# Kernel optimization log

Measured on AMD Instinct MI355X. Metric: run time of the kernel, lower is better.

Reference implementation:

```python
import jax, jax.numpy as jnp
import numpy as np

N, E, D_IN, HID, OUT, EDIM, L, NT, ET = 50000, 800000, 128, 128, 128, 32, 3, 2, 3
PUMP = 1
LN_EPS = 1e-5


def setup_inputs() -> dict:
    key = jax.random.key(0)
    ks = jax.random.split(key, 12)
    s = 0.05
    x = jax.random.normal(ks[0], (N, D_IN), jnp.float32)
    edge_index = jax.random.randint(ks[1], (2, E), 0, N, dtype=jnp.int64)
    edge_attr = jax.random.normal(ks[2], (E, EDIM), jnp.float32)
    node_type = jax.random.randint(ks[3], (N,), 0, NT, dtype=jnp.int64)
    edge_type = jax.random.randint(ks[4], (E,), 0, ET, dtype=jnp.int64)
    # per-layer HydroConv params
    node_W = jax.random.normal(ks[5], (L, NT, HID, D_IN), jnp.float32) * s   # per-node-type Linear weight
    node_b = jax.random.normal(ks[6], (L, NT, HID), jnp.float32) * s
    edge_W = jax.random.normal(ks[7], (L, ET, 2, EDIM), jnp.float32) * s     # out dim padded to 2; row 1 only used for pump type
    edge_b = jax.random.normal(ks[8], (L, ET, 2), jnp.float32) * s
    emb = jax.random.normal(ks[9], (L, ET, EDIM), jnp.float32) * s           # edge_type_emb per layer
    ln_g = jnp.ones((L, HID), jnp.float32)
    ln_b = jnp.zeros((L, HID), jnp.float32)
    fc_W = jax.random.normal(ks[10], (OUT, HID), jnp.float32) * s
    fc_b = jnp.zeros((OUT,), jnp.float32)
    return dict(x=x, edge_attr=edge_attr, node_W=node_W, node_b=node_b,
                edge_W=edge_W, edge_b=edge_b, emb=emb, ln_g=ln_g, ln_b=ln_b,
                fc_W=fc_W, fc_b=fc_b, edge_index=edge_index,
                node_type=node_type, edge_type=edge_type)


def _hydro_conv(h, edge_index, edge_attr, node_type, edge_type, nW, nb, eW, eb, emb_l):
    src, dst = edge_index[0], edge_index[1]           # x_j = h[src], x_i = h[dst]
    direction = edge_attr[:, -2:-1]                    # [E,1]
    pump = edge_attr[:, -1:]                           # [E,1]
    ea = edge_attr + emb_l[edge_type]                  # [E,EDIM]
    raw = jnp.einsum('ec,toc->eto', ea, eW) + eb       # [E,ET,2]
    raw = jnp.take_along_axis(raw, edge_type[:, None, None], axis=1)[:, 0]  # [E,2] per-edge-type MLP
    gain = jax.nn.softplus(raw[:, :1])                 # [E,1]
    speed = pump * jnp.where(direction > 0, direction, jnp.ones_like(direction))
    is_pump = (edge_type == PUMP)[:, None]
    gain = jnp.where(is_pump, gain * speed, gain)
    bias = jnp.where(is_pump, raw[:, 1:2] * speed, jnp.zeros_like(gain))
    sign = direction * 2.0 - 1.0
    msg = sign * (gain * (h[src] - h[dst]) + bias)     # [E,C]
    aggr = jax.ops.segment_sum(msg, dst, num_segments=N)  # scatter-add to target nodes
    out = jnp.zeros((N, nW.shape[1]), h.dtype)
    for t in range(NT):                                # per-node-type Linear
        ht = aggr @ nW[t].T + nb[t]
        out = jnp.where((node_type == t)[:, None], ht, out)
    return out


def reference(x, edge_attr, node_W, node_b, edge_W, edge_b, emb, ln_g, ln_b,
              fc_W, fc_b, edge_index, node_type, edge_type):
    h = x
    for l in range(L):
        identity = h
        h = _hydro_conv(h, edge_index, edge_attr, node_type, edge_type,
                        node_W[l], node_b[l], edge_W[l], edge_b[l], emb[l])
        h = jax.nn.relu(h)
        mu = jnp.mean(h, axis=-1, keepdims=True)
        var = jnp.mean(jnp.square(h - mu), axis=-1, keepdims=True)
        h = (h - mu) * jax.lax.rsqrt(var + LN_EPS) * ln_g[l] + ln_b[l]
        if identity.shape == h.shape:                  # residual
            h = h + identity
    return h @ fc_W.T + fc_b
```

## Files before the change

kernel.cpp:

```cpp
#include <hip/hip_runtime.h>
#include <math.h>

#define NN 50000
#define EE 800000
#define D 128
#define EDIM 32
#define LL 3
#define NT 2
#define ET 3
#define NB 196
#define NPAD 50080
#define NTILE 1565
#define NBLKM 392

typedef _Float16 f16x8 __attribute__((ext_vector_type(8)));
typedef float f32x4 __attribute__((ext_vector_type(4)));

__device__ __forceinline__ void cvt8(const float4 u, const float4 v, f16x8& hi, f16x8& lo) {
    float x[8] = {u.x, u.y, u.z, u.w, v.x, v.y, v.z, v.w};
#pragma unroll
    for (int e = 0; e < 8; e++) {
        _Float16 h = (_Float16)x[e];
        hi[e] = h;
        lo[e] = (_Float16)(x[e] - (float)h);
    }
}

__global__ __launch_bounds__(256) void k_pcount(const int* __restrict__ nt, int* __restrict__ pc) {
    __shared__ int s[256];
    int d = blockIdx.x * 256 + threadIdx.x;
    int ind = 0;
    if (d < NN) ind = (nt[d] == 0) ? 1 : 0x10000;
    s[threadIdx.x] = ind;
    __syncthreads();
    for (int st = 128; st; st >>= 1) {
        if (threadIdx.x < st) s[threadIdx.x] += s[threadIdx.x + st];
        __syncthreads();
    }
    if (threadIdx.x == 0) pc[blockIdx.x] = s[0];
}

__global__ __launch_bounds__(256) void k_pscan(const int* __restrict__ pc, int* __restrict__ po,
                                               int* __restrict__ meta) {
    __shared__ int s[256];
    int t = threadIdx.x;
    int v = (t < NB) ? pc[t] : 0;
    s[t] = v;
    __syncthreads();
    for (int st = 1; st < 256; st <<= 1) {
        int add = (t >= st) ? s[t - st] : 0;
        __syncthreads();
        s[t] += add;
        __syncthreads();
    }
    if (t < NB) po[t] = s[t] - v;
    if (t == 0) {
        int tot = s[255];
        meta[3] = ((tot & 0xffff) + 63) & ~63;
    }
}

__global__ __launch_bounds__(256) void k_passign(const int* __restrict__ nt, const int* __restrict__ po,
                                                 const int* __restrict__ meta,
                                                 int* __restrict__ pos, int* __restrict__ inv) {
    __shared__ int s[256];
    int t = threadIdx.x;
    int d = blockIdx.x * 256 + t;
    int ty = (d < NN) ? nt[d] : -1;
    int ind = (ty == 0) ? 1 : ((ty == 1) ? 0x10000 : 0);
    s[t] = ind;
    __syncthreads();
    for (int st = 1; st < 256; st <<= 1) {
        int add = (t >= st) ? s[t - st] : 0;
        __syncthreads();
        s[t] += add;
        __syncthreads();
    }
    if (d >= NN) return;
    int excl = s[t] - ind;
    int pop = po[blockIdx.x];
    int p;
    if (ty == 0) p = (pop & 0xffff) + (excl & 0xffff);
    else         p = meta[3] + (pop >> 16) + (excl >> 16);
    pos[d] = p;
    inv[p] = d;
}

__global__ __launch_bounds__(256) void k_permx(const float* __restrict__ x, const int* __restrict__ pos,
                                               float* __restrict__ h0) {
    int flat = blockIdx.x * 256 + threadIdx.x;
    if (flat >= NN * 32) return;
    int d = flat >> 5, f4 = flat & 31;
    int p = pos[d];
    ((float4*)h0)[(size_t)p * 32 + f4] = ((const float4*)x)[(size_t)d * 32 + f4];
}

__global__ __launch_bounds__(256) void k_hist(const int* __restrict__ dst, int* __restrict__ deg) {
    int e = blockIdx.x * 256 + threadIdx.x;
    if (e < EE) atomicAdd(&deg[dst[e]], 1);
}

__global__ __launch_bounds__(256) void k_scan_bsum(const int* __restrict__ deg, int* __restrict__ bsum) {
    __shared__ int s[256];
    int t = threadIdx.x;
    int d = blockIdx.x * 256 + t;
    s[t] = (d < NN) ? deg[d] : 0;
    __syncthreads();
    for (int st = 128; st > 0; st >>= 1) {
        if (t < st) s[t] += s[t + st];
        __syncthreads();
    }
    if (t == 0) bsum[blockIdx.x] = s[0];
}

__global__ __launch_bounds__(256) void k_scan_boff(const int* __restrict__ bsum, int* __restrict__ boff) {
    __shared__ int s[256];
    int t = threadIdx.x;
    s[t] = (t < NB) ? bsum[t] : 0;
    __syncthreads();
    for (int st = 1; st < 256; st <<= 1) {
        int add = (t >= st) ? s[t - st] : 0;
        __syncthreads();
        s[t] += add;
        __syncthreads();
    }
    if (t < NB) boff[t] = (t == 0) ? 0 : s[t - 1];
}

__global__ __launch_bounds__(256) void k_scan_offs(const int* __restrict__ deg, const int* __restrict__ boff,
                                                   int* __restrict__ offs, int* __restrict__ cur) {
    __shared__ int s[256];
    int t = threadIdx.x;
    int d = blockIdx.x * 256 + t;
    int v = (d < NN) ? deg[d] : 0;
    s[t] = v;
    __syncthreads();
    for (int st = 1; st < 256; st <<= 1) {
        int add = (t >= st) ? s[t - st] : 0;
        __syncthreads();
        s[t] += add;
        __syncthreads();
    }
    if (d < NN) {
        int excl = s[t] - v + boff[blockIdx.x];
        offs[d] = excl;
        cur[d]  = excl;
    }
}

__global__ __launch_bounds__(256) void k_edge(const float* __restrict__ edge_attr,
                                              const float* __restrict__ edge_W,
                                              const float* __restrict__ edge_b,
                                              const float* __restrict__ emb,
                                              const int* __restrict__ ei,
                                              const int* __restrict__ etype,
                                              const int* __restrict__ pos,
                                              int* __restrict__ cur,
                                              float4* __restrict__ esort) {
    __shared__ float eWl[LL * ET * 2 * EDIM];
    __shared__ float ebd[LL * ET * 2];
    int t0 = threadIdx.x;
    for (int i = t0; i < LL * ET * 2 * EDIM; i += 256) eWl[i] = edge_W[i];
    __syncthreads();
    if (t0 < LL * ET * 2) {
        int l = t0 / (ET * 2);
        int rem = t0 % (ET * 2);
        int tt = rem / 2;
        float sum = edge_b[t0];
        const float* em = emb + (l * ET + tt) * EDIM;
        const float* w  = eWl + t0 * EDIM;
        for (int c = 0; c < EDIM; c++) sum += em[c] * w[c];
        ebd[t0] = sum;
    }
    __syncthreads();
    int e = blockIdx.x * 256 + t0;
    if (e >= EE) return;

    float a[EDIM];
    const float4* ap = (const float4*)(edge_attr + (size_t)e * EDIM);
#pragma unroll
    for (int i = 0; i < EDIM / 4; i++) {
        float4 v = ap[i];
        a[4 * i + 0] = v.x; a[4 * i + 1] = v.y; a[4 * i + 2] = v.z; a[4 * i + 3] = v.w;
    }
    int tt = etype[e];
    float dir  = a[EDIM - 2];
    float pump = a[EDIM - 1];
    float sign = dir * 2.f - 1.f;
    float speed = pump * (dir > 0.f ? dir : 1.f);
    int src = ei[e];
    int dst = ei[EE + e];
    int sp = pos[src];
    int p = atomicAdd(&cur[dst], 1);
    float Av[LL], Bv[LL];
#pragma unroll
    for (int l = 0; l < LL; l++) {
        const float* w0 = eWl + ((l * ET + tt) * 2 + 0) * EDIM;
        const float* w1 = w0 + EDIM;
        float r0 = ebd[(l * ET + tt) * 2 + 0];
        float r1 = ebd[(l * ET + tt) * 2 + 1];
#pragma unroll
        for (int c = 0; c < EDIM; c++) { r0 += a[c] * w0[c]; r1 += a[c] * w1[c]; }
        float gain = fmaxf(r0, 0.f) + log1pf(expf(-fabsf(r0)));
        float bias = 0.f;
        if (tt == 1) { gain *= speed; bias = r1 * speed; }
        Av[l] = sign * gain;
        Bv[l] = sign * bias;
    }
    float4 e0 = make_float4(__int_as_float(sp), Av[0], Av[1], Av[2]);
    float4 e1 = make_float4(Bv[0], Bv[1], Bv[2], 0.f);
    esort[(size_t)p * 2 + 0] = e0;
    esort[(size_t)p * 2 + 1] = e1;
}

__global__ __launch_bounds__(256) void k_gather(const float* __restrict__ h,
                                                const int* __restrict__ offs,
                                                const int* __restrict__ deg,
                                                const int* __restrict__ pos,
                                                const float4* __restrict__ esort,
                                                int layer,
                                                float* __restrict__ aggr) {
    __shared__ float4 rbuf[2][32];
    __shared__ float  rsum[2][2];
    int local = threadIdx.x;
    int nb = local >> 7;
    int node = blockIdx.x * 2 + nb;
    int t = local & 127;
    int w = t >> 5;
    int f4 = t & 31;
    int start = offs[node];
    int n = deg[node];
    int p = pos[node];

    float4 acc = make_float4(0.f, 0.f, 0.f, 0.f);
    float sA = 0.f, sB = 0.f;
    for (int k = w; k < n; k += 4) {
        size_t idx = (size_t)(start + k) * 2;
        float4 e0 = esort[idx];
        float4 e1 = esort[idx + 1];
        int sp = __float_as_int(e0.x);
        float A = (layer == 0) ? e0.y : ((layer == 1) ? e0.z : e0.w);
        float B = (layer == 0) ? e1.x : ((layer == 1) ? e1.y : e1.z);
        float4 hv = *(const float4*)&h[(size_t)sp * D + 4 * f4];
        acc.x += A * hv.x; acc.y += A * hv.y; acc.z += A * hv.z; acc.w += A * hv.w;
        sA += A; sB += B;
    }
    acc.x += __shfl_xor(acc.x, 32); acc.y += __shfl_xor(acc.y, 32);
    acc.z += __shfl_xor(acc.z, 32); acc.w += __shfl_xor(acc.w, 32);
    sA += __shfl_xor(sA, 32); sB += __shfl_xor(sB, 32);
    if (((local >> 6) & 1) == 1 && (t & 63) < 32) {
        rbuf[nb][f4] = acc;
        if (f4 == 0) { rsum[nb][0] = sA; rsum[nb][1] = sB; }
    }
    __syncthreads();
    if (((local >> 6) & 1) == 0 && (t & 63) < 32) {
        float4 o = rbuf[nb][f4];
        float sAt = sA + rsum[nb][0];
        float sBt = sB + rsum[nb][1];
        float4 hd = *(const float4*)&h[(size_t)p * D + 4 * f4];
        float4 r;
        r.x = acc.x + o.x - sAt * hd.x + sBt;
        r.y = acc.y + o.y - sAt * hd.y + sBt;
        r.z = acc.z + o.z - sAt * hd.z + sBt;
        r.w = acc.w + o.w - sAt * hd.w + sBt;
        *(float4*)&aggr[(size_t)p * D + 4 * f4] = r;
    }
}

__global__ __launch_bounds__(256) void k_node(const float* __restrict__ aggr,
                                              const float* __restrict__ hprev,
                                              const float* __restrict__ Wg,
                                              const float* __restrict__ bg,
                                              const float* __restrict__ lng,
                                              const float* __restrict__ lnb,
                                              const int* __restrict__ meta,
                                              float* __restrict__ hnext) {
    int wid  = threadIdx.x >> 6;
    int lane = threadIdx.x & 63;
    int w0 = (blockIdx.x * 4 + wid) * 32;
    if (w0 >= NPAD) return;
    int l15 = lane & 15, lg = lane >> 4;
    int tt = (w0 >= meta[3]) ? 1 : 0;
    const float* W = Wg + (size_t)tt * D * D;

    f32x4 acc[2][8];
#pragma unroll
    for (int i = 0; i < 2; i++)
#pragma unroll
        for (int j = 0; j < 8; j++) acc[i][j] = (f32x4){0.f, 0.f, 0.f, 0.f};

#pragma unroll 1
    for (int ks = 0; ks < 4; ks++) {
        int kb = ks * 32 + 8 * lg;
        float4 rA[2][2], rB[8][2];
#pragma unroll
        for (int i = 0; i < 2; i++) {
            const float* p = aggr + (size_t)(w0 + 16 * i + l15) * D + kb;
            rA[i][0] = *(const float4*)p;
            rA[i][1] = *(const float4*)(p + 4);
        }
#pragma unroll
        for (int j = 0; j < 8; j++) {
            const float* p = W + (size_t)(16 * j + l15) * D + kb;
            rB[j][0] = *(const float4*)p;
            rB[j][1] = *(const float4*)(p + 4);
        }
        f16x8 ahi[2], alo[2];
#pragma unroll
        for (int i = 0; i < 2; i++) cvt8(rA[i][0], rA[i][1], ahi[i], alo[i]);
#pragma unroll
        for (int j = 0; j < 8; j++) {
            f16x8 bhi, blo;
            cvt8(rB[j][0], rB[j][1], bhi, blo);
#pragma unroll
            for (int i = 0; i < 2; i++) {
                acc[i][j] = __builtin_amdgcn_mfma_f32_16x16x32_f16(ahi[i], bhi, acc[i][j], 0, 0, 0);
                acc[i][j] = __builtin_amdgcn_mfma_f32_16x16x32_f16(alo[i], bhi, acc[i][j], 0, 0, 0);
                acc[i][j] = __builtin_amdgcn_mfma_f32_16x16x32_f16(ahi[i], blo, acc[i][j], 0, 0, 0);
            }
        }
    }

    float bv[8], gv[8], bb[8];
#pragma unroll
    for (int j = 0; j < 8; j++) {
        int col = 16 * j + l15;
        bv[j] = bg[tt * D + col];
        gv[j] = lng[col];
        bb[j] = lnb[col];
    }
#pragma unroll
    for (int i = 0; i < 2; i++)
#pragma unroll
        for (int j = 0; j < 8; j++)
#pragma unroll
            for (int r = 0; r < 4; r++)
                acc[i][j][r] = fmaxf(acc[i][j][r] + bv[j], 0.f);

    float mu[2][4], rs[2][4];
#pragma unroll
    for (int i = 0; i < 2; i++)
#pragma unroll
        for (int r = 0; r < 4; r++) {
            float s = 0.f, s2 = 0.f;
#pragma unroll
            for (int j = 0; j < 8; j++) { float v = acc[i][j][r]; s += v; s2 += v * v; }
#pragma unroll
            for (int m = 1; m < 16; m <<= 1) { s += __shfl_xor(s, m); s2 += __shfl_xor(s2, m); }
            float mm = s * (1.f / 128.f);
            mu[i][r] = mm;
            rs[i][r] = rsqrtf(s2 * (1.f / 128.f) - mm * mm + 1e-5f);
        }

#pragma unroll
    for (int i = 0; i < 2; i++)
#pragma unroll
        for (int r = 0; r < 4; r++) {
            int row = w0 + 16 * i + 4 * lg + r;
#pragma unroll
            for (int j = 0; j < 8; j++) {
                int col = 16 * j + l15;
                float v = (acc[i][j][r] - mu[i][r]) * rs[i][r] * gv[j] + bb[j]
                          + hprev[(size_t)row * D + col];
                hnext[(size_t)row * D + col] = v;
            }
        }
}

__global__ __launch_bounds__(256) void k_fc(const float* __restrict__ hin,
                                            const float* __restrict__ W,
                                            const float* __restrict__ bias,
                                            const int* __restrict__ inv,
                                            float* __restrict__ out) {
    int wid  = threadIdx.x >> 6;
    int lane = threadIdx.x & 63;
    int w0 = (blockIdx.x * 4 + wid) * 32;
    if (w0 >= NPAD) return;
    int l15 = lane & 15, lg = lane >> 4;

    f32x4 acc[2][8];
#pragma unroll
    for (int i = 0; i < 2; i++)
#pragma unroll
        for (int j = 0; j < 8; j++) acc[i][j] = (f32x4){0.f, 0.f, 0.f, 0.f};

#pragma unroll 1
    for (int ks = 0; ks < 4; ks++) {
        int kb = ks * 32 + 8 * lg;
        float4 rA[2][2], rB[8][2];
#pragma unroll
        for (int i = 0; i < 2; i++) {
            const float* p = hin + (size_t)(w0 + 16 * i + l15) * D + kb;
            rA[i][0] = *(const float4*)p;
            rA[i][1] = *(const float4*)(p + 4);
        }
#pragma unroll
        for (int j = 0; j < 8; j++) {
            const float* p = W + (size_t)(16 * j + l15) * D + kb;
            rB[j][0] = *(const float4*)p;
            rB[j][1] = *(const float4*)(p + 4);
        }
        f16x8 ahi[2], alo[2];
#pragma unroll
        for (int i = 0; i < 2; i++) cvt8(rA[i][0], rA[i][1], ahi[i], alo[i]);
#pragma unroll
        for (int j = 0; j < 8; j++) {
            f16x8 bhi, blo;
            cvt8(rB[j][0], rB[j][1], bhi, blo);
#pragma unroll
            for (int i = 0; i < 2; i++) {
                acc[i][j] = __builtin_amdgcn_mfma_f32_16x16x32_f16(ahi[i], bhi, acc[i][j], 0, 0, 0);
                acc[i][j] = __builtin_amdgcn_mfma_f32_16x16x32_f16(alo[i], bhi, acc[i][j], 0, 0, 0);
                acc[i][j] = __builtin_amdgcn_mfma_f32_16x16x32_f16(ahi[i], blo, acc[i][j], 0, 0, 0);
            }
        }
    }

    float bv[8];
#pragma unroll
    for (int j = 0; j < 8; j++) bv[j] = bias[16 * j + l15];

#pragma unroll
    for (int i = 0; i < 2; i++)
#pragma unroll
        for (int r = 0; r < 4; r++) {
            int row = w0 + 16 * i + 4 * lg + r;
            int orig = inv[row];
            if (orig >= 0) {
#pragma unroll
                for (int j = 0; j < 8; j++)
                    out[(size_t)orig * D + 16 * j + l15] = acc[i][j][r] + bv[j];
            }
        }
}

extern "C" void kernel_launch(void* const* d_in, const int* in_sizes, int n_in,
                              void* d_out, int out_size, void* d_ws, size_t ws_size,
                              hipStream_t stream) {
    const float* x         = (const float*)d_in[0];
    const float* edge_attr = (const float*)d_in[1];
    const float* node_W    = (const float*)d_in[2];
    const float* node_b    = (const float*)d_in[3];
    const float* edge_W    = (const float*)d_in[4];
    const float* edge_b    = (const float*)d_in[5];
    const float* emb       = (const float*)d_in[6];
    const float* ln_g      = (const float*)d_in[7];
    const float* ln_b      = (const float*)d_in[8];
    const float* fc_W      = (const float*)d_in[9];
    const float* fc_b      = (const float*)d_in[10];
    const int*   edge_index = (const int*)d_in[11];
    const int*   node_type  = (const int*)d_in[12];
    const int*   edge_type  = (const int*)d_in[13];
    float* out = (float*)d_out;

    char* w = (char*)d_ws;
    auto alloc = [&](size_t bytes) {
        void* p = (void*)w;
        w += (bytes + 255) & ~(size_t)255;
        return p;
    };
    float*  P     = (float*)alloc((size_t)NPAD * D * 4);
    float*  Q     = (float*)alloc((size_t)NPAD * D * 4);
    float*  G     = (float*)alloc((size_t)NPAD * D * 4);
    float4* esort = (float4*)alloc((size_t)EE * 32);
    int*    pos   = (int*)alloc((size_t)NN * 4);
    int*    inv   = (int*)alloc((size_t)NPAD * 4);
    int*    deg   = (int*)alloc((size_t)NN * 4);
    int*    offs  = (int*)alloc((size_t)NN * 4);
    int*    cur   = (int*)alloc((size_t)NN * 4);
    int*    bsum  = (int*)alloc(256 * 4);
    int*    boff  = (int*)alloc(256 * 4);
    int*    pc    = (int*)alloc(256 * 4);
    int*    po    = (int*)alloc(256 * 4);
    int*    meta  = (int*)alloc(8 * 4);

    hipMemsetAsync(deg, 0, (size_t)NN * 4, stream);
    hipMemsetAsync(inv, 0xFF, (size_t)NPAD * 4, stream);

    k_pcount<<<NB, 256, 0, stream>>>(node_type, pc);
    k_pscan<<<1, 256, 0, stream>>>(pc, po, meta);
    k_passign<<<NB, 256, 0, stream>>>(node_type, po, meta, pos, inv);
    k_permx<<<(NN * 32 + 255) / 256, 256, 0, stream>>>(x, pos, P);

    k_hist<<<(EE + 255) / 256, 256, 0, stream>>>(edge_index + EE, deg);
    k_scan_bsum<<<NB, 256, 0, stream>>>(deg, bsum);
    k_scan_boff<<<1, 256, 0, stream>>>(bsum, boff);
    k_scan_offs<<<NB, 256, 0, stream>>>(deg, boff, offs, cur);
    k_edge<<<(EE + 255) / 256, 256, 0, stream>>>(edge_attr, edge_W, edge_b, emb,
                                                 edge_index, edge_type, pos, cur, esort);

    const float* hin = P;
    float* outs[LL] = {Q, P, Q};
    for (int l = 0; l < LL; l++) {
        k_gather<<<NN / 2, 256, 0, stream>>>(hin, offs, deg, pos, esort, l, G);
        k_node<<<NBLKM, 256, 0, stream>>>(G, hin,
                                          node_W + (size_t)l * NT * D * D,
                                          node_b + (size_t)l * NT * D,
                                          ln_g + (size_t)l * D,
                                          ln_b + (size_t)l * D,
                                          meta, outs[l]);
        hin = outs[l];
    }
    k_fc<<<NBLKM, 256, 0, stream>>>(hin, fc_W, fc_b, inv, out);
}
```

Before: 595.5 us.

## Shrink edge records, pre-reduce per-node bias, unroll gather loads

The per-edge bias term is now summed per destination node with atomics in the edge kernel, so each sorted edge record shrinks from two float4 to one. The gather loop is unrolled four ways, issuing independent edge and neighbour-row loads before accumulating, to add memory-level parallelism. The edge kernel handles two edges per thread and pads its shared weight rows to 33 floats to avoid bank conflicts. The cost is float atomics on pump edges plus an extra memset and buffer, and atomic ordering makes the bias sum nondeterministic.

```diff
diff --git a/kernel.cpp b/kernel.cpp
--- a/kernel.cpp
+++ b/kernel.cpp
@@ -156,61 +156,101 @@
                                               const int* __restrict__ etype,
                                               const int* __restrict__ pos,
                                               int* __restrict__ cur,
-                                              float4* __restrict__ esort) {
-    __shared__ float eWl[LL * ET * 2 * EDIM];
-    __shared__ float ebd[LL * ET * 2];
+                                              float4* __restrict__ esort,
+                                              float* __restrict__ sBn) {
+    __shared__ float eWl[18 * 33];
+    __shared__ float ebd[18];
     int t0 = threadIdx.x;
-    for (int i = t0; i < LL * ET * 2 * EDIM; i += 256) eWl[i] = edge_W[i];
-    __syncthreads();
-    if (t0 < LL * ET * 2) {
+    for (int i = t0; i < 18 * EDIM; i += 256) eWl[(i >> 5) * 33 + (i & 31)] = edge_W[i];
+    __syncthreads();
+    if (t0 < 18) {
         int l = t0 / (ET * 2);
         int rem = t0 % (ET * 2);
         int tt = rem / 2;
         float sum = edge_b[t0];
         const float* em = emb + (l * ET + tt) * EDIM;
-        const float* w  = eWl + t0 * EDIM;
-        for (int c = 0; c < EDIM; c++) sum += em[c] * w[c];
+        const float* wq = eWl + t0 * 33;
+        for (int c = 0; c < EDIM; c++) sum += em[c] * wq[c];
         ebd[t0] = sum;
     }
     __syncthreads();
-    int e = blockIdx.x * 256 + t0;
-    if (e >= EE) return;
-
-    float a[EDIM];
-    const float4* ap = (const float4*)(edge_attr + (size_t)e * EDIM);
-#pragma unroll
-    for (int i = 0; i < EDIM / 4; i++) {
-        float4 v = ap[i];
-        a[4 * i + 0] = v.x; a[4 * i + 1] = v.y; a[4 * i + 2] = v.z; a[4 * i + 3] = v.w;
-    }
-    int tt = etype[e];
-    float dir  = a[EDIM - 2];
-    float pump = a[EDIM - 1];
-    float sign = dir * 2.f - 1.f;
-    float speed = pump * (dir > 0.f ? dir : 1.f);
-    int src = ei[e];
-    int dst = ei[EE + e];
-    int sp = pos[src];
-    int p = atomicAdd(&cur[dst], 1);
-    float Av[LL], Bv[LL];
+
+    int eA = blockIdx.x * 512 + t0;
+    int eB = eA + 256;
+    bool vA = (eA < EE);
+    bool vB = (eB < EE);
+    int eAc = vA ? eA : 0;
+    int eBc = vB ? eB : eAc;
+
+    float a0[EDIM], a1[EDIM];
+    {
+        const float4* ap = (const float4*)(edge_attr + (size_t)eAc * EDIM);
+#pragma unroll
+        for (int i = 0; i < EDIM / 4; i++) {
+            float4 v = ap[i];
+            a0[4 * i + 0] = v.x; a0[4 * i + 1] = v.y; a0[4 * i + 2] = v.z; a0[4 * i + 3] = v.w;
+        }
+    }
+    {
+        const float4* ap = (const float4*)(edge_attr + (size_t)eBc * EDIM);
+#pragma unroll
+        for (int i = 0; i < EDIM / 4; i++) {
+            float4 v = ap[i];
+            a1[4 * i + 0] = v.x; a1[4 * i + 1] = v.y; a1[4 * i + 2] = v.z; a1[4 * i + 3] = v.w;
+        }
+    }
+    int ttA = etype[eAc],   ttB = etype[eBc];
+    int srcA = ei[eAc],     srcB = ei[eBc];
+    int dstA = ei[EE + eAc], dstB = ei[EE + eBc];
+    int spA = pos[srcA],    spB = pos[srcB];
+    int pA = vA ? atomicAdd(&cur[dstA], 1) : 0;
+    int pB = vB ? atomicAdd(&cur[dstB], 1) : 0;
+
+    float dirA = a0[EDIM - 2], pumpA = a0[EDIM - 1];
+    float dirB = a1[EDIM - 2], pumpB = a1[EDIM - 1];
+    float signA = dirA * 2.f - 1.f, signB = dirB * 2.f - 1.f;
+    float speedA = pumpA * (dirA > 0.f ? dirA : 1.f);
+    float speedB = pumpB * (dirB > 0.f ? dirB : 1.f);
+
+    float AvA[LL], BvA[LL], AvB[LL], BvB[LL];
 #pragma unroll
     for (int l = 0; l < LL; l++) {
-        const float* w0 = eWl + ((l * ET + tt) * 2 + 0) * EDIM;
-        const float* w1 = w0 + EDIM;
-        float r0 = ebd[(l * ET + tt) * 2 + 0];
-        float r1 = ebd[(l * ET + tt) * 2 + 1];
-#pragma unroll
-        for (int c = 0; c < EDIM; c++) { r0 += a[c] * w0[c]; r1 += a[c] * w1[c]; }
-        float gain = fmaxf(r0, 0.f) + log1pf(expf(-fabsf(r0)));
-        float bias = 0.f;
-        if (tt == 1) { gain *= speed; bias = r1 * speed; }
-        Av[l] = sign * gain;
-        Bv[l] = sign * bias;
-    }
-    float4 e0 = make_float4(__int_as_float(sp), Av[0], Av[1], Av[2]);
-    float4 e1 = make_float4(Bv[0], Bv[1], Bv[2], 0.f);
-    esort[(size_t)p * 2 + 0] = e0;
-    esort[(size_t)p * 2 + 1] = e1;
+        const float* w0A = eWl + ((l * ET + ttA) * 2 + 0) * 33;
+        const float* w1A = w0A + 33;
+        const float* w0B = eWl + ((l * ET + ttB) * 2 + 0) * 33;
+        const float* w1B = w0B + 33;
+        float r0A = ebd[(l * ET + ttA) * 2 + 0];
+        float r1A = ebd[(l * ET + ttA) * 2 + 1];
+        float r0B = ebd[(l * ET + ttB) * 2 + 0];
+        float r1B = ebd[(l * ET + ttB) * 2 + 1];
+#pragma unroll
+        for (int c = 0; c < EDIM; c++) {
+            r0A += a0[c] * w0A[c]; r1A += a0[c] * w1A[c];
+            r0B += a1[c] * w0B[c]; r1B += a1[c] * w1B[c];
+        }
+        float gA = fmaxf(r0A, 0.f) + log1pf(expf(-fabsf(r0A)));
+        float gB = fmaxf(r0B, 0.f) + log1pf(expf(-fabsf(r0B)));
+        float biA = 0.f, biB = 0.f;
+        if (ttA == 1) { gA *= speedA; biA = r1A * speedA; }
+        if (ttB == 1) { gB *= speedB; biB = r1B * speedB; }
+        AvA[l] = signA * gA; BvA[l] = signA * biA;
+        AvB[l] = signB * gB; BvB[l] = signB * biB;
+    }
+
+    if (vA) {
+        esort[pA] = make_float4(__int_as_float(spA), AvA[0], AvA[1], AvA[2]);
+        if (ttA == 1) {
+#pragma unroll
+            for (int l = 0; l < LL; l++) atomicAdd(&sBn[l * NN + dstA], BvA[l]);
+        }
+    }
+    if (vB) {
+        esort[pB] = make_float4(__int_as_float(spB), AvB[0], AvB[1], AvB[2]);
+        if (ttB == 1) {
+#pragma unroll
+            for (int l = 0; l < LL; l++) atomicAdd(&sBn[l * NN + dstB], BvB[l]);
+        }
+    }
 }
 
 __global__ __launch_bounds__(256) void k_gather(const float* __restrict__ h,
@@ -218,10 +258,11 @@
                                                 const int* __restrict__ deg,
                                                 const int* __restrict__ pos,
                                                 const float4* __restrict__ esort,
+                                                const float* __restrict__ sBn,
                                                 int layer,
                                                 float* __restrict__ aggr) {
     __shared__ float4 rbuf[2][32];
-    __shared__ float  rsum[2][2];
+    __shared__ float  rsum[2];
     int local = threadIdx.x;
     int nb = local >> 7;
     int node = blockIdx.x * 2 + nb;
@@ -233,30 +274,42 @@
     int p = pos[node];
 
     float4 acc = make_float4(0.f, 0.f, 0.f, 0.f);
-    float sA = 0.f, sB = 0.f;
-    for (int k = w; k < n; k += 4) {
-        size_t idx = (size_t)(start + k) * 2;
-        float4 e0 = esort[idx];
-        float4 e1 = esort[idx + 1];
-        int sp = __float_as_int(e0.x);
-        float A = (layer == 0) ? e0.y : ((layer == 1) ? e0.z : e0.w);
-        float B = (layer == 0) ? e1.x : ((layer == 1) ? e1.y : e1.z);
-        float4 hv = *(const float4*)&h[(size_t)sp * D + 4 * f4];
-        acc.x += A * hv.x; acc.y += A * hv.y; acc.z += A * hv.z; acc.w += A * hv.w;
-        sA += A; sB += B;
+    float sA = 0.f;
+    for (int k = w; k < n; k += 16) {
+        float4 e[4];
+#pragma unroll
+        for (int u = 0; u < 4; u++) {
+            int ku = k + 4 * u;
+            e[u] = esort[(ku < n) ? (size_t)(start + ku) : (size_t)start];
+        }
+        float4 hv[4];
+#pragma unroll
+        for (int u = 0; u < 4; u++) {
+            int s = __float_as_int(e[u].x);
+            hv[u] = *(const float4*)&h[(size_t)s * D + 4 * f4];
+        }
+#pragma unroll
+        for (int u = 0; u < 4; u++) {
+            int ku = k + 4 * u;
+            float A = (layer == 0) ? e[u].y : ((layer == 1) ? e[u].z : e[u].w);
+            if (ku >= n) A = 0.f;
+            acc.x += A * hv[u].x; acc.y += A * hv[u].y;
+            acc.z += A * hv[u].z; acc.w += A * hv[u].w;
+            sA += A;
+        }
     }
     acc.x += __shfl_xor(acc.x, 32); acc.y += __shfl_xor(acc.y, 32);
     acc.z += __shfl_xor(acc.z, 32); acc.w += __shfl_xor(acc.w, 32);
-    sA += __shfl_xor(sA, 32); sB += __shfl_xor(sB, 32);
+    sA += __shfl_xor(sA, 32);
     if (((local >> 6) & 1) == 1 && (t & 63) < 32) {
         rbuf[nb][f4] = acc;
-        if (f4 == 0) { rsum[nb][0] = sA; rsum[nb][1] = sB; }
+        if (f4 == 0) rsum[nb] = sA;
     }
     __syncthreads();
     if (((local >> 6) & 1) == 0 && (t & 63) < 32) {
         float4 o = rbuf[nb][f4];
-        float sAt = sA + rsum[nb][0];
-        float sBt = sB + rsum[nb][1];
+        float sAt = sA + rsum[nb];
+        float sBt = sBn[layer * NN + node];
         float4 hd = *(const float4*)&h[(size_t)p * D + 4 * f4];
         float4 r;
         r.x = acc.x + o.x - sAt * hd.x + sBt;
@@ -462,7 +515,8 @@
     float*  P     = (float*)alloc((size_t)NPAD * D * 4);
     float*  Q     = (float*)alloc((size_t)NPAD * D * 4);
     float*  G     = (float*)alloc((size_t)NPAD * D * 4);
-    float4* esort = (float4*)alloc((size_t)EE * 32);
+    float4* esort = (float4*)alloc((size_t)EE * 16);
+    float*  sBn   = (float*)alloc((size_t)LL * NN * 4);
     int*    pos   = (int*)alloc((size_t)NN * 4);
     int*    inv   = (int*)alloc((size_t)NPAD * 4);
     int*    deg   = (int*)alloc((size_t)NN * 4);
@@ -476,6 +530,7 @@
 
     hipMemsetAsync(deg, 0, (size_t)NN * 4, stream);
     hipMemsetAsync(inv, 0xFF, (size_t)NPAD * 4, stream);
+    hipMemsetAsync(sBn, 0, (size_t)LL * NN * 4, stream);
 
     k_pcount<<<NB, 256, 0, stream>>>(node_type, pc);
     k_pscan<<<1, 256, 0, stream>>>(pc, po, meta);
@@ -486,13 +541,13 @@
     k_scan_bsum<<<NB, 256, 0, stream>>>(deg, bsum);
     k_scan_boff<<<1, 256, 0, stream>>>(bsum, boff);
     k_scan_offs<<<NB, 256, 0, stream>>>(deg, boff, offs, cur);
-    k_edge<<<(EE + 255) / 256, 256, 0, stream>>>(edge_attr, edge_W, edge_b, emb,
-                                                 edge_index, edge_type, pos, cur, esort);
+    k_edge<<<(EE + 511) / 512, 256, 0, stream>>>(edge_attr, edge_W, edge_b, emb,
+                                                 edge_index, edge_type, pos, cur, esort, sBn);
 
     const float* hin = P;
     float* outs[LL] = {Q, P, Q};
     for (int l = 0; l < LL; l++) {
-        k_gather<<<NN / 2, 256, 0, stream>>>(hin, offs, deg, pos, esort, l, G);
+        k_gather<<<NN / 2, 256, 0, stream>>>(hin, offs, deg, pos, esort, sBn, l, G);
         k_node<<<NBLKM, 256, 0, stream>>>(G, hin,
                                           node_W + (size_t)l * NT * D * D,
                                           node_b + (size_t)l * NT * D,
```

Result: no change. 606.3 us (+1.8%).

## Reuse histogram atomic ranks for CSR placement, pad edge weights, batch gather loads

Applied to the files above, without the earlier changes.

The histogram kernel now stores each edge's atomic return value as its rank, so the edge kernel computes its sorted slot as offs[dst]+rank without a second round of atomics on a cursor array. The per-edge weights in shared memory are padded to a stride of 33, which is meant to reduce bank conflicts. The gather loop is unrolled four ways, issuing four edge-record loads and then four feature-row loads before accumulating, so more memory requests are in flight per wave. The cost is an extra E-sized rank buffer and higher register pressure in the gather kernel.

```diff
diff --git a/kernel.cpp b/kernel.cpp
--- a/kernel.cpp
+++ b/kernel.cpp
@@ -95,9 +95,13 @@
     ((float4*)h0)[(size_t)p * 32 + f4] = ((const float4*)x)[(size_t)d * 32 + f4];
 }
 
-__global__ __launch_bounds__(256) void k_hist(const int* __restrict__ dst, int* __restrict__ deg) {
+__global__ __launch_bounds__(256) void k_hist(const int* __restrict__ dst, int* __restrict__ deg,
+                                              int* __restrict__ rank) {
     int e = blockIdx.x * 256 + threadIdx.x;
-    if (e < EE) atomicAdd(&deg[dst[e]], 1);
+    if (e < EE) {
+        int r = atomicAdd(&deg[dst[e]], 1);
+        rank[e] = r;
+    }
 }
 
 __global__ __launch_bounds__(256) void k_scan_bsum(const int* __restrict__ deg, int* __restrict__ bsum) {
@@ -128,7 +132,7 @@
 }
 
 __global__ __launch_bounds__(256) void k_scan_offs(const int* __restrict__ deg, const int* __restrict__ boff,
-                                                   int* __restrict__ offs, int* __restrict__ cur) {
+                                                   int* __restrict__ offs) {
     __shared__ int s[256];
     int t = threadIdx.x;
     int d = blockIdx.x * 256 + t;
@@ -141,11 +145,7 @@
         s[t] += add;
         __syncthreads();
     }
-    if (d < NN) {
-        int excl = s[t] - v + boff[blockIdx.x];
-        offs[d] = excl;
-        cur[d]  = excl;
-    }
+    if (d < NN) offs[d] = s[t] - v + boff[blockIdx.x];
 }
 
 __global__ __launch_bounds__(256) void k_edge(const float* __restrict__ edge_attr,
@@ -155,21 +155,22 @@
                                               const int* __restrict__ ei,
                                               const int* __restrict__ etype,
                                               const int* __restrict__ pos,
-                                              int* __restrict__ cur,
+                                              const int* __restrict__ offs,
+                                              const int* __restrict__ rank,
                                               float4* __restrict__ esort) {
-    __shared__ float eWl[LL * ET * 2 * EDIM];
-    __shared__ float ebd[LL * ET * 2];
+    __shared__ float eWl[18 * 33];
+    __shared__ float ebd[18];
     int t0 = threadIdx.x;
-    for (int i = t0; i < LL * ET * 2 * EDIM; i += 256) eWl[i] = edge_W[i];
-    __syncthreads();
-    if (t0 < LL * ET * 2) {
+    for (int i = t0; i < 18 * EDIM; i += 256) eWl[(i >> 5) * 33 + (i & 31)] = edge_W[i];
+    __syncthreads();
+    if (t0 < 18) {
         int l = t0 / (ET * 2);
         int rem = t0 % (ET * 2);
         int tt = rem / 2;
         float sum = edge_b[t0];
         const float* em = emb + (l * ET + tt) * EDIM;
-        const float* w  = eWl + t0 * EDIM;
-        for (int c = 0; c < EDIM; c++) sum += em[c] * w[c];
+        const float* wq  = eWl + t0 * 33;
+        for (int c = 0; c < EDIM; c++) sum += em[c] * wq[c];
         ebd[t0] = sum;
     }
     __syncthreads();
@@ -191,12 +192,12 @@
     int src = ei[e];
     int dst = ei[EE + e];
     int sp = pos[src];
-    int p = atomicAdd(&cur[dst], 1);
+    int p = offs[dst] + rank[e];
     float Av[LL], Bv[LL];
 #pragma unroll
     for (int l = 0; l < LL; l++) {
-        const float* w0 = eWl + ((l * ET + tt) * 2 + 0) * EDIM;
-        const float* w1 = w0 + EDIM;
+        const float* w0 = eWl + ((l * ET + tt) * 2 + 0) * 33;
+        const float* w1 = w0 + 33;
         float r0 = ebd[(l * ET + tt) * 2 + 0];
         float r1 = ebd[(l * ET + tt) * 2 + 1];
 #pragma unroll
@@ -234,16 +235,31 @@
 
     float4 acc = make_float4(0.f, 0.f, 0.f, 0.f);
     float sA = 0.f, sB = 0.f;
-    for (int k = w; k < n; k += 4) {
-        size_t idx = (size_t)(start + k) * 2;
-        float4 e0 = esort[idx];
-        float4 e1 = esort[idx + 1];
-        int sp = __float_as_int(e0.x);
-        float A = (layer == 0) ? e0.y : ((layer == 1) ? e0.z : e0.w);
-        float B = (layer == 0) ? e1.x : ((layer == 1) ? e1.y : e1.z);
-        float4 hv = *(const float4*)&h[(size_t)sp * D + 4 * f4];
-        acc.x += A * hv.x; acc.y += A * hv.y; acc.z += A * hv.z; acc.w += A * hv.w;
-        sA += A; sB += B;
+    for (int k = w; k < n; k += 16) {
+        float4 e0[4], e1[4];
+#pragma unroll
+        for (int u = 0; u < 4; u++) {
+            int ku = k + 4 * u;
+            size_t idx = (ku < n) ? (size_t)(start + ku) * 2 : (size_t)start * 2;
+            e0[u] = esort[idx];
+            e1[u] = esort[idx + 1];
+        }
+        float4 hv[4];
+#pragma unroll
+        for (int u = 0; u < 4; u++) {
+            int s = __float_as_int(e0[u].x);
+            hv[u] = *(const float4*)&h[(size_t)s * D + 4 * f4];
+        }
+#pragma unroll
+        for (int u = 0; u < 4; u++) {
+            int ku = k + 4 * u;
+            float A = (layer == 0) ? e0[u].y : ((layer == 1) ? e0[u].z : e0[u].w);
+            float B = (layer == 0) ? e1[u].x : ((layer == 1) ? e1[u].y : e1[u].z);
+            if (ku >= n) { A = 0.f; B = 0.f; }
+            acc.x += A * hv[u].x; acc.y += A * hv[u].y;
+            acc.z += A * hv[u].z; acc.w += A * hv[u].w;
+            sA += A; sB += B;
+        }
     }
     acc.x += __shfl_xor(acc.x, 32); acc.y += __shfl_xor(acc.y, 32);
     acc.z += __shfl_xor(acc.z, 32); acc.w += __shfl_xor(acc.w, 32);
@@ -463,11 +479,11 @@
     float*  Q     = (float*)alloc((size_t)NPAD * D * 4);
     float*  G     = (float*)alloc((size_t)NPAD * D * 4);
     float4* esort = (float4*)alloc((size_t)EE * 32);
+    int*    rank  = (int*)alloc((size_t)EE * 4);
     int*    pos   = (int*)alloc((size_t)NN * 4);
     int*    inv   = (int*)alloc((size_t)NPAD * 4);
     int*    deg   = (int*)alloc((size_t)NN * 4);
     int*    offs  = (int*)alloc((size_t)NN * 4);
-    int*    cur   = (int*)alloc((size_t)NN * 4);
     int*    bsum  = (int*)alloc(256 * 4);
     int*    boff  = (int*)alloc(256 * 4);
     int*    pc    = (int*)alloc(256 * 4);
@@ -482,12 +498,12 @@
     k_passign<<<NB, 256, 0, stream>>>(node_type, po, meta, pos, inv);
     k_permx<<<(NN * 32 + 255) / 256, 256, 0, stream>>>(x, pos, P);
 
-    k_hist<<<(EE + 255) / 256, 256, 0, stream>>>(edge_index + EE, deg);
+    k_hist<<<(EE + 255) / 256, 256, 0, stream>>>(edge_index + EE, deg, rank);
     k_scan_bsum<<<NB, 256, 0, stream>>>(deg, bsum);
     k_scan_boff<<<1, 256, 0, stream>>>(bsum, boff);
-    k_scan_offs<<<NB, 256, 0, stream>>>(deg, boff, offs, cur);
+    k_scan_offs<<<NB, 256, 0, stream>>>(deg, boff, offs);
     k_edge<<<(EE + 255) / 256, 256, 0, stream>>>(edge_attr, edge_W, edge_b, emb,
-                                                 edge_index, edge_type, pos, cur, esort);
+                                                 edge_index, edge_type, pos, offs, rank, esort);
 
     const float* hin = P;
     float* outs[LL] = {Q, P, Q};
```

Result: no change. 586.3 us (-1.5%).
